# Performance work log

Hardware: AMD Instinct MI355X
Metric: run time of the kernel (lower is better)

## Reference

```python
import jax, jax.numpy as jnp
from jax import lax
import numpy as np

VOCAB, EMB, HID = 6, 64, 64


def _glorot(key, shape):
    fan_in, fan_out = shape[0], shape[-1]
    lim = np.sqrt(6.0 / (fan_in + fan_out)).astype(np.float32)
    return jax.random.uniform(key, shape, jnp.float32, -lim, lim)


def setup_inputs() -> dict:
    key = jax.random.key(0)
    ks = jax.random.split(key, 10)
    B, T = 256, 2048
    tokens = jax.random.randint(ks[0], (B, T), 0, VOCAB, dtype=jnp.int32)
    emb = jax.random.normal(ks[1], (VOCAB, EMB), jnp.float32) * 0.05  # Keras uniform init approx
    # LSTM kernels: gate order i, f, c(g), o ; kernel [EMB,4H], recurrent [H,4H], bias [4H]
    W_f = _glorot(ks[2], (EMB, 4 * HID))
    U_f = _glorot(ks[3], (HID, 4 * HID))
    b_f = jnp.zeros((4 * HID,), jnp.float32).at[HID:2 * HID].set(1.0)  # unit_forget_bias
    W_b = _glorot(ks[4], (EMB, 4 * HID))
    U_b = _glorot(ks[5], (HID, 4 * HID))
    b_b = jnp.zeros((4 * HID,), jnp.float32).at[HID:2 * HID].set(1.0)
    W_d = _glorot(ks[6], (2 * HID, 1))
    b_d = jnp.zeros((1,), jnp.float32)
    return {"tokens": tokens, "emb": emb, "W_f": W_f, "U_f": U_f, "b_f": b_f,
            "W_b": W_b, "U_b": U_b, "b_b": b_b, "W_d": W_d, "b_d": b_d}


def _masked_lstm(x, mask, W, U, b):
    """x: [B,T,E] float, mask: [B,T] bool. Returns [B,T,H].
    Keras mask semantics: at masked steps, state AND output carry previous values."""
    B = x.shape[0]
    h0 = jnp.zeros((B, HID), x.dtype)
    c0 = jnp.zeros((B, HID), x.dtype)

    def step(carry, inp):
        h, c = carry
        xt, mt = inp  # [B,E], [B]
        z = xt @ W + h @ U + b  # [B,4H]
        i, f, g, o = jnp.split(z, 4, axis=-1)
        c_new = jax.nn.sigmoid(f) * c + jax.nn.sigmoid(i) * jnp.tanh(g)
        h_new = jax.nn.sigmoid(o) * jnp.tanh(c_new)
        m = mt[:, None]
        h2 = jnp.where(m, h_new, h)
        c2 = jnp.where(m, c_new, c)
        return (h2, c2), h2

    xs = (jnp.swapaxes(x, 0, 1), jnp.swapaxes(mask, 0, 1))  # time-major
    _, hs = lax.scan(step, (h0, c0), xs)
    return jnp.swapaxes(hs, 0, 1)  # [B,T,H]


def reference(tokens, emb, W_f, U_f, b_f, W_b, U_b, b_b, W_d, b_d):
    mask = tokens != 0  # mask_zero=True
    x = emb[tokens]  # [B,T,EMB]
    fwd = _masked_lstm(x, mask, W_f, U_f, b_f)
    # backward direction: reverse inputs and mask in time, run, reverse outputs back
    bwd = _masked_lstm(x[:, ::-1], mask[:, ::-1], W_b, U_b, b_b)[:, ::-1]
    seq = jnp.concatenate([fwd, bwd], axis=-1)  # [B,T,2H]
    last = seq[:, -1, :]
    return last @ W_d + b_d  # [B,1]
```

## Files before the change

### kernel.cpp

```cpp
#include <hip/hip_runtime.h>


#define TT 2048
#define L2E 1.4426950408889634f

__device__ __forceinline__ float fexp2(float x) { return __builtin_amdgcn_exp2f(x); }
__device__ __forceinline__ float frcp(float x)  { return __builtin_amdgcn_rcpf(x); }
__device__ __forceinline__ float fsigm(float x) { return frcp(1.f + fexp2(-L2E * x)); }
__device__ __forceinline__ float ftanh(float x) { return fmaf(2.f, frcp(1.f + fexp2(-2.f * L2E * x)), -1.f); }
__device__ __forceinline__ float readlane_f(float v, int l) {
  return __builtin_bit_cast(float, __builtin_amdgcn_readlane(__builtin_bit_cast(int, v), l));
}

__global__ void
__attribute__((amdgpu_flat_work_group_size(256, 256)))
__attribute__((amdgpu_waves_per_eu(1, 1)))
lstm_fused(
    const int* __restrict__ tokens,
    const float* __restrict__ emb,
    const float* __restrict__ W_f, const float* __restrict__ U_f, const float* __restrict__ b_f,
    const float* __restrict__ W_b, const float* __restrict__ b_b,
    const float* __restrict__ W_d, const float* __restrict__ b_d,
    float* __restrict__ out)
{
  const int b    = blockIdx.x;
  const int tid  = threadIdx.x;
  const int lane = tid & 63;
  const int g    = tid >> 6;

  __shared__ int   tok_s [TT + 8];
  __shared__ int   ctok_s[TT + 8];
  __shared__ float emb_s[6 * 64];
  __shared__ float zx_s [6 * 272];
  __shared__ float zxb_s[6 * 256];
  __shared__ float act_s[2][4 * 68];
  __shared__ int   wsum[4];

  {
    const int4* tsrc = (const int4*)(tokens + b * TT);
    int4* tdst = (int4*)tok_s;
    for (int i = tid; i < TT / 4; i += 256) tdst[i] = tsrc[i];
    if (tid < 8) { tok_s[TT + tid] = 0; ctok_s[TT + tid] = 0; }
    for (int i = tid; i < 384; i += 256) emb_s[i] = emb[i];
  }
  __syncthreads();

  int mytok[8];
  int cnt = 0;
#pragma unroll
  for (int j = 0; j < 8; ++j) {
    mytok[j] = tok_s[tid * 8 + j];
    cnt += (mytok[j] != 0);
  }
  int inc = cnt;
#pragma unroll
  for (int off = 1; off < 64; off <<= 1) {
    int v = __shfl_up(inc, off, 64);
    if (lane >= off) inc += v;
  }
  if (lane == 63) wsum[g] = inc;
  __syncthreads();
  int base = 0;
#pragma unroll
  for (int w = 0; w < 4; ++w) base += (w < g) ? wsum[w] : 0;
  int pos = base + inc - cnt;
#pragma unroll
  for (int j = 0; j < 8; ++j)
    if (mytok[j] != 0) ctok_s[pos++] = mytok[j];
  const int nact = __builtin_amdgcn_readfirstlane(wsum[0] + wsum[1] + wsum[2] + wsum[3]);

  {
    float af[6], ab[6];
#pragma unroll
    for (int v = 0; v < 6; ++v) { af[v] = b_f[tid]; ab[v] = b_b[tid]; }
    for (int e = 0; e < 64; ++e) {
      const float wf = W_f[e * 256 + tid];
      const float wb = W_b[e * 256 + tid];
#pragma unroll
      for (int v = 0; v < 6; ++v) {
        af[v] = fmaf(emb_s[v * 64 + e], wf, af[v]);
        ab[v] = fmaf(emb_s[v * 64 + e], wb, ab[v]);
      }
    }
#pragma unroll
    for (int v = 0; v < 6; ++v) {
      zx_s [v * 272 + g * 68 + lane] = af[v];
      zxb_s[v * 256 + tid] = ab[v];
    }
  }

  float Ucol[64];
#pragma unroll
  for (int k = 0; k < 64; ++k) Ucol[k] = U_f[k * 256 + tid];

  __syncthreads();

  const float m1 = (g == 2) ? (-2.f * L2E) : (-L2E);
  const float ya = (g == 2) ? 2.f : 1.f;
  const float yb = (g == 2) ? -1.f : 0.f;
  const int   goff = g * 68 + lane;

  float h_reg = 0.f, c_reg = 0.f;
  int   buf = 0;
  int   tokc = ctok_s[0];

  for (int s = 0; s < nact; ++s) {
    const int tokn = ctok_s[s + 1];
    const float zxv = zx_s[tokc * 272 + goff];
    float a0 = 0.f, a1 = 0.f, a2 = 0.f, a3 = 0.f;
#pragma unroll
    for (int k = 0; k < 64; k += 4) {
      a0 = fmaf(readlane_f(h_reg, k + 0), Ucol[k + 0], a0);
      a1 = fmaf(readlane_f(h_reg, k + 1), Ucol[k + 1], a1);
      a2 = fmaf(readlane_f(h_reg, k + 2), Ucol[k + 2], a2);
      a3 = fmaf(readlane_f(h_reg, k + 3), Ucol[k + 3], a3);
    }
    const float z = zxv + ((a0 + a1) + (a2 + a3));
    const float y = fmaf(ya, frcp(1.f + fexp2(z * m1)), yb);
    act_s[buf][goff] = y;
    __syncthreads();
    const float ai  = act_s[buf][lane];
    const float af2 = act_s[buf][68 + lane];
    const float ag  = act_s[buf][136 + lane];
    const float ao  = act_s[buf][204 + lane];
    c_reg = fmaf(af2, c_reg, ai * ag);
    h_reg = ao * ftanh(c_reg);
    buf ^= 1;
    tokc = tokn;
  }

  if (tid < 64) {
    const float hf   = h_reg;
    const int   tokL = tok_s[TT - 1];
    float hbv = 0.f;
    if (tokL != 0) {
      const float zi = zxb_s[tokL * 256 + tid];
      const float zg = zxb_s[tokL * 256 + 128 + tid];
      const float zo = zxb_s[tokL * 256 + 192 + tid];
      const float cn = fsigm(zi) * ftanh(zg);
      hbv = fsigm(zo) * ftanh(cn);
    }
    float pr = fmaf(hf, W_d[tid], hbv * W_d[64 + tid]);
#pragma unroll
    for (int off = 32; off > 0; off >>= 1) pr += __shfl_xor(pr, off, 64);
    if (tid == 0) out[b] = pr + b_d[0];
  }
}

extern "C" void kernel_launch(void* const* d_in, const int* in_sizes, int n_in,
                              void* d_out, int out_size, void* d_ws, size_t ws_size,
                              hipStream_t stream) {
  const int*   tokens = (const int*)d_in[0];
  const float* emb    = (const float*)d_in[1];
  const float* W_f    = (const float*)d_in[2];
  const float* U_f    = (const float*)d_in[3];
  const float* b_f    = (const float*)d_in[4];
  const float* W_b    = (const float*)d_in[5];
  const float* U_b    = (const float*)d_in[6];
  (void)U_b;
  const float* b_b    = (const float*)d_in[7];
  const float* W_d    = (const float*)d_in[8];
  const float* b_d    = (const float*)d_in[9];
  float* out = (float*)d_out;
  (void)d_ws; (void)ws_size;

  lstm_fused<<<256, 256, 0, stream>>>(tokens, emb, W_f, U_f, b_f, W_b, b_b,
                                      W_d, b_d, out);
}
```

Baseline: 770.1 us.

## Run each sequence's LSTM recurrence in a single wave without barriers

Moves each batch row from four waves (one per gate) to a single 64-lane wave. Each lane now computes all four gates for its hidden unit, using packed v2f FMAs over 128 U values held in registers. This removes the per-step __syncthreads and the LDS exchange of activations, and lets the per-step input projection be read as one float4. The cost is roughly four times the FMA work per lane per step and much higher register pressure (256 VGPRs for U), which could cause spills, while only one wave per CU is busy.

```diff
diff --git a/kernel.cpp b/kernel.cpp
--- a/kernel.cpp
+++ b/kernel.cpp
@@ -3,6 +3,8 @@
 
 #define TT 2048
 #define L2E 1.4426950408889634f
+
+typedef float v2f __attribute__((ext_vector_type(2)));
 
 __device__ __forceinline__ float fexp2(float x) { return __builtin_amdgcn_exp2f(x); }
 __device__ __forceinline__ float frcp(float x)  { return __builtin_amdgcn_rcpf(x); }
@@ -13,7 +15,7 @@
 }
 
 __global__ void
-__attribute__((amdgpu_flat_work_group_size(256, 256)))
+__attribute__((amdgpu_flat_work_group_size(64, 64)))
 __attribute__((amdgpu_waves_per_eu(1, 1)))
 lstm_fused(
     const int* __restrict__ tokens,
@@ -23,59 +25,49 @@
     const float* __restrict__ W_d, const float* __restrict__ b_d,
     float* __restrict__ out)
 {
-  const int b    = blockIdx.x;
-  const int tid  = threadIdx.x;
-  const int lane = tid & 63;
-  const int g    = tid >> 6;
+  const int b = blockIdx.x;
+  const int u = threadIdx.x;
 
-  __shared__ int   tok_s [TT + 8];
+  __shared__ int   tok_s [TT];
   __shared__ int   ctok_s[TT + 8];
   __shared__ float emb_s[6 * 64];
-  __shared__ float zx_s [6 * 272];
-  __shared__ float zxb_s[6 * 256];
-  __shared__ float act_s[2][4 * 68];
-  __shared__ int   wsum[4];
+  __shared__ float zx_s [6 * 256] __attribute__((aligned(16)));
+  __shared__ float zxb_s[6 * 256] __attribute__((aligned(16)));
 
   {
     const int4* tsrc = (const int4*)(tokens + b * TT);
     int4* tdst = (int4*)tok_s;
-    for (int i = tid; i < TT / 4; i += 256) tdst[i] = tsrc[i];
-    if (tid < 8) { tok_s[TT + tid] = 0; ctok_s[TT + tid] = 0; }
-    for (int i = tid; i < 384; i += 256) emb_s[i] = emb[i];
+    for (int i = u; i < TT / 4; i += 64) tdst[i] = tsrc[i];
+    for (int i = u; i < 384; i += 64) emb_s[i] = emb[i];
   }
   __syncthreads();
 
-  int mytok[8];
   int cnt = 0;
-#pragma unroll
-  for (int j = 0; j < 8; ++j) {
-    mytok[j] = tok_s[tid * 8 + j];
-    cnt += (mytok[j] != 0);
-  }
+  for (int j = 0; j < 32; ++j) cnt += (tok_s[u * 32 + j] != 0);
   int inc = cnt;
 #pragma unroll
   for (int off = 1; off < 64; off <<= 1) {
     int v = __shfl_up(inc, off, 64);
-    if (lane >= off) inc += v;
+    if (u >= off) inc += v;
   }
-  if (lane == 63) wsum[g] = inc;
+  int pos = inc - cnt;
+  for (int j = 0; j < 32; ++j) {
+    const int t = tok_s[u * 32 + j];
+    if (t != 0) ctok_s[pos++] = t;
+  }
+  const int nact = __builtin_amdgcn_readfirstlane(__shfl(inc, 63, 64));
+  if (u < 8) ctok_s[nact + u] = 0;
   __syncthreads();
-  int base = 0;
+
 #pragma unroll
-  for (int w = 0; w < 4; ++w) base += (w < g) ? wsum[w] : 0;
-  int pos = base + inc - cnt;
-#pragma unroll
-  for (int j = 0; j < 8; ++j)
-    if (mytok[j] != 0) ctok_s[pos++] = mytok[j];
-  const int nact = __builtin_amdgcn_readfirstlane(wsum[0] + wsum[1] + wsum[2] + wsum[3]);
-
-  {
+  for (int g4 = 0; g4 < 4; ++g4) {
+    const int col = g4 * 64 + u;
     float af[6], ab[6];
 #pragma unroll
-    for (int v = 0; v < 6; ++v) { af[v] = b_f[tid]; ab[v] = b_b[tid]; }
+    for (int v = 0; v < 6; ++v) { af[v] = b_f[col]; ab[v] = b_b[col]; }
     for (int e = 0; e < 64; ++e) {
-      const float wf = W_f[e * 256 + tid];
-      const float wb = W_b[e * 256 + tid];
+      const float wf = W_f[e * 256 + col];
+      const float wb = W_b[e * 256 + col];
 #pragma unroll
       for (int v = 0; v < 6; ++v) {
         af[v] = fmaf(emb_s[v * 64 + e], wf, af[v]);
@@ -84,67 +76,57 @@
     }
 #pragma unroll
     for (int v = 0; v < 6; ++v) {
-      zx_s [v * 272 + g * 68 + lane] = af[v];
-      zxb_s[v * 256 + tid] = ab[v];
+      zx_s [v * 256 + u * 4 + g4] = af[v];
+      zxb_s[v * 256 + u * 4 + g4] = ab[v];
     }
   }
 
-  float Ucol[64];
+  v2f U01[64], U23[64];
 #pragma unroll
-  for (int k = 0; k < 64; ++k) Ucol[k] = U_f[k * 256 + tid];
+  for (int k = 0; k < 64; ++k) {
+    U01[k] = v2f{U_f[k * 256 + u],       U_f[k * 256 + 64 + u]};
+    U23[k] = v2f{U_f[k * 256 + 128 + u], U_f[k * 256 + 192 + u]};
+  }
 
   __syncthreads();
 
-  const float m1 = (g == 2) ? (-2.f * L2E) : (-L2E);
-  const float ya = (g == 2) ? 2.f : 1.f;
-  const float yb = (g == 2) ? -1.f : 0.f;
-  const int   goff = g * 68 + lane;
-
   float h_reg = 0.f, c_reg = 0.f;
-  int   buf = 0;
-  int   tokc = ctok_s[0];
+  int tokc = ctok_s[0];
 
   for (int s = 0; s < nact; ++s) {
     const int tokn = ctok_s[s + 1];
-    const float zxv = zx_s[tokc * 272 + goff];
-    float a0 = 0.f, a1 = 0.f, a2 = 0.f, a3 = 0.f;
+    const float4 zx4 = *(const float4*)&zx_s[tokc * 256 + u * 4];
+    v2f a01 = v2f{zx4.x, zx4.y}, a23 = v2f{zx4.z, zx4.w};
+    v2f b01 = v2f{0.f, 0.f},     b23 = v2f{0.f, 0.f};
 #pragma unroll
-    for (int k = 0; k < 64; k += 4) {
-      a0 = fmaf(readlane_f(h_reg, k + 0), Ucol[k + 0], a0);
-      a1 = fmaf(readlane_f(h_reg, k + 1), Ucol[k + 1], a1);
-      a2 = fmaf(readlane_f(h_reg, k + 2), Ucol[k + 2], a2);
-      a3 = fmaf(readlane_f(h_reg, k + 3), Ucol[k + 3], a3);
+    for (int k = 0; k < 64; k += 2) {
+      const float h0 = readlane_f(h_reg, k);
+      const float h1 = readlane_f(h_reg, k + 1);
+      a01 += U01[k] * h0;       a23 += U23[k] * h0;
+      b01 += U01[k + 1] * h1;   b23 += U23[k + 1] * h1;
     }
-    const float z = zxv + ((a0 + a1) + (a2 + a3));
-    const float y = fmaf(ya, frcp(1.f + fexp2(z * m1)), yb);
-    act_s[buf][goff] = y;
-    __syncthreads();
-    const float ai  = act_s[buf][lane];
-    const float af2 = act_s[buf][68 + lane];
-    const float ag  = act_s[buf][136 + lane];
-    const float ao  = act_s[buf][204 + lane];
-    c_reg = fmaf(af2, c_reg, ai * ag);
-    h_reg = ao * ftanh(c_reg);
-    buf ^= 1;
+    const v2f z01 = a01 + b01;
+    const v2f z23 = a23 + b23;
+    const float yi = fsigm(z01.x);
+    const float yf = fsigm(z01.y);
+    const float yg = ftanh(z23.x);
+    const float yo = fsigm(z23.y);
+    c_reg = fmaf(yf, c_reg, yi * yg);
+    h_reg = yo * ftanh(c_reg);
     tokc = tokn;
   }
 
-  if (tid < 64) {
-    const float hf   = h_reg;
-    const int   tokL = tok_s[TT - 1];
-    float hbv = 0.f;
-    if (tokL != 0) {
-      const float zi = zxb_s[tokL * 256 + tid];
-      const float zg = zxb_s[tokL * 256 + 128 + tid];
-      const float zo = zxb_s[tokL * 256 + 192 + tid];
-      const float cn = fsigm(zi) * ftanh(zg);
-      hbv = fsigm(zo) * ftanh(cn);
-    }
-    float pr = fmaf(hf, W_d[tid], hbv * W_d[64 + tid]);
+  const int tokL = tok_s[TT - 1];
+  float hbv = 0.f;
+  if (tokL != 0) {
+    const float4 zb = *(const float4*)&zxb_s[tokL * 256 + u * 4];
+    const float cn = fsigm(zb.x) * ftanh(zb.z);
+    hbv = fsigm(zb.w) * ftanh(cn);
+  }
+  float pr = fmaf(h_reg, W_d[u], hbv * W_d[64 + u]);
 #pragma unroll
-    for (int off = 32; off > 0; off >>= 1) pr += __shfl_xor(pr, off, 64);
-    if (tid == 0) out[b] = pr + b_d[0];
-  }
+  for (int off = 32; off > 0; off >>= 1) pr += __shfl_xor(pr, off, 64);
+  if (u == 0) out[b] = pr + b_d[0];
 }
 
 extern "C" void kernel_launch(void* const* d_in, const int* in_sizes, int n_in,
@@ -164,6 +146,6 @@
   float* out = (float*)d_out;
   (void)d_ws; (void)ws_size;
 
-  lstm_fused<<<256, 256, 0, stream>>>(tokens, emb, W_f, U_f, b_f, W_b, b_b,
-                                      W_d, b_d, out);
+  lstm_fused<<<256, 64, 0, stream>>>(tokens, emb, W_f, U_f, b_f, W_b, b_b,
+                                     W_d, b_d, out);
 }
```

Result: slower. 1.328 ms (+72.4%).

## Remap LSTM gates within each wave and exchange activations via shuffles

Applied to the files above, without the earlier changes.

Each wave now owns 16 hidden units for all four gates instead of one gate for all 64 units. Gate activations are combined with in-wave shuffles, and only the new hidden state goes through LDS. This replaces the 256-float activation exchange and the redundant per-wave cell update with a 64-float h exchange, still behind one barrier per step. Readlanes are also batched into 16-wide buffers to overlap them with FMAs, which adds three cross-lane shuffles on the serial dependency chain.

```diff
diff --git a/kernel.cpp b/kernel.cpp
--- a/kernel.cpp
+++ b/kernel.cpp
@@ -11,6 +11,26 @@
 __device__ __forceinline__ float readlane_f(float v, int l) {
   return __builtin_bit_cast(float, __builtin_amdgcn_readlane(__builtin_bit_cast(int, v), l));
 }
+
+#define RL16(B, base)                                                             \
+  B[0]  = readlane_f(h_reg, (base) + 0);  B[1]  = readlane_f(h_reg, (base) + 1);  \
+  B[2]  = readlane_f(h_reg, (base) + 2);  B[3]  = readlane_f(h_reg, (base) + 3);  \
+  B[4]  = readlane_f(h_reg, (base) + 4);  B[5]  = readlane_f(h_reg, (base) + 5);  \
+  B[6]  = readlane_f(h_reg, (base) + 6);  B[7]  = readlane_f(h_reg, (base) + 7);  \
+  B[8]  = readlane_f(h_reg, (base) + 8);  B[9]  = readlane_f(h_reg, (base) + 9);  \
+  B[10] = readlane_f(h_reg, (base) + 10); B[11] = readlane_f(h_reg, (base) + 11); \
+  B[12] = readlane_f(h_reg, (base) + 12); B[13] = readlane_f(h_reg, (base) + 13); \
+  B[14] = readlane_f(h_reg, (base) + 14); B[15] = readlane_f(h_reg, (base) + 15);
+
+#define FMA16(B, base)                                                       \
+  a0 = fmaf(B[0],  Ucol[(base) + 0],  a0); a1 = fmaf(B[1],  Ucol[(base) + 1],  a1); \
+  a2 = fmaf(B[2],  Ucol[(base) + 2],  a2); a3 = fmaf(B[3],  Ucol[(base) + 3],  a3); \
+  a0 = fmaf(B[4],  Ucol[(base) + 4],  a0); a1 = fmaf(B[5],  Ucol[(base) + 5],  a1); \
+  a2 = fmaf(B[6],  Ucol[(base) + 6],  a2); a3 = fmaf(B[7],  Ucol[(base) + 7],  a3); \
+  a0 = fmaf(B[8],  Ucol[(base) + 8],  a0); a1 = fmaf(B[9],  Ucol[(base) + 9],  a1); \
+  a2 = fmaf(B[10], Ucol[(base) + 10], a2); a3 = fmaf(B[11], Ucol[(base) + 11], a3); \
+  a0 = fmaf(B[12], Ucol[(base) + 12], a0); a1 = fmaf(B[13], Ucol[(base) + 13], a1); \
+  a2 = fmaf(B[14], Ucol[(base) + 14], a2); a3 = fmaf(B[15], Ucol[(base) + 15], a3);
 
 __global__ void
 __attribute__((amdgpu_flat_work_group_size(256, 256)))
@@ -26,14 +46,18 @@
   const int b    = blockIdx.x;
   const int tid  = threadIdx.x;
   const int lane = tid & 63;
-  const int g    = tid >> 6;
+  const int w    = tid >> 6;
+  const int g    = lane >> 4;
+  const int ul   = lane & 15;
+  const int u    = 16 * w + ul;
+  const int col  = (g << 6) + u;
 
   __shared__ int   tok_s [TT + 8];
   __shared__ int   ctok_s[TT + 8];
   __shared__ float emb_s[6 * 64];
   __shared__ float zx_s [6 * 272];
   __shared__ float zxb_s[6 * 256];
-  __shared__ float act_s[2][4 * 68];
+  __shared__ float h_s[2][64];
   __shared__ int   wsum[4];
 
   {
@@ -42,6 +66,7 @@
     for (int i = tid; i < TT / 4; i += 256) tdst[i] = tsrc[i];
     if (tid < 8) { tok_s[TT + tid] = 0; ctok_s[TT + tid] = 0; }
     for (int i = tid; i < 384; i += 256) emb_s[i] = emb[i];
+    if (tid < 64) { h_s[0][tid] = 0.f; h_s[1][tid] = 0.f; }
   }
   __syncthreads();
 
@@ -58,11 +83,11 @@
     int v = __shfl_up(inc, off, 64);
     if (lane >= off) inc += v;
   }
-  if (lane == 63) wsum[g] = inc;
+  if (lane == 63) wsum[w] = inc;
   __syncthreads();
   int base = 0;
 #pragma unroll
-  for (int w = 0; w < 4; ++w) base += (w < g) ? wsum[w] : 0;
+  for (int ww = 0; ww < 4; ++ww) base += (ww < w) ? wsum[ww] : 0;
   int pos = base + inc - cnt;
 #pragma unroll
   for (int j = 0; j < 8; ++j)
@@ -84,23 +109,24 @@
     }
 #pragma unroll
     for (int v = 0; v < 6; ++v) {
-      zx_s [v * 272 + g * 68 + lane] = af[v];
+      zx_s [v * 272 + (tid >> 6) * 68 + (tid & 63)] = af[v];
       zxb_s[v * 256 + tid] = ab[v];
     }
   }
 
   float Ucol[64];
 #pragma unroll
-  for (int k = 0; k < 64; ++k) Ucol[k] = U_f[k * 256 + tid];
+  for (int k = 0; k < 64; ++k) Ucol[k] = U_f[k * 256 + col];
 
   __syncthreads();
 
   const float m1 = (g == 2) ? (-2.f * L2E) : (-L2E);
   const float ya = (g == 2) ? 2.f : 1.f;
   const float yb = (g == 2) ? -1.f : 0.f;
-  const int   goff = g * 68 + lane;
+  const int   goff = g * 68 + u;
 
-  float h_reg = 0.f, c_reg = 0.f;
+  float h_reg = 0.f;
+  float c_reg = 0.f;
   int   buf = 0;
   int   tokc = ctok_s[0];
 
@@ -108,24 +134,26 @@
     const int tokn = ctok_s[s + 1];
     const float zxv = zx_s[tokc * 272 + goff];
     float a0 = 0.f, a1 = 0.f, a2 = 0.f, a3 = 0.f;
-#pragma unroll
-    for (int k = 0; k < 64; k += 4) {
-      a0 = fmaf(readlane_f(h_reg, k + 0), Ucol[k + 0], a0);
-      a1 = fmaf(readlane_f(h_reg, k + 1), Ucol[k + 1], a1);
-      a2 = fmaf(readlane_f(h_reg, k + 2), Ucol[k + 2], a2);
-      a3 = fmaf(readlane_f(h_reg, k + 3), Ucol[k + 3], a3);
-    }
+    float hsA[16], hsB[16];
+    RL16(hsA, 0)
+    RL16(hsB, 16)
+    FMA16(hsA, 0)
+    RL16(hsA, 32)
+    FMA16(hsB, 16)
+    RL16(hsB, 48)
+    FMA16(hsA, 32)
+    FMA16(hsB, 48)
     const float z = zxv + ((a0 + a1) + (a2 + a3));
     const float y = fmaf(ya, frcp(1.f + fexp2(z * m1)), yb);
-    act_s[buf][goff] = y;
+    const float vf = __shfl(y, ul + 16, 64);
+    const float vg = __shfl(y, ul + 32, 64);
+    const float vo = __shfl(y, ul + 48, 64);
+    c_reg = fmaf(vf, c_reg, y * vg);
+    const float hn = vo * ftanh(c_reg);
+    if (lane < 16) h_s[buf ^ 1][u] = hn;
     __syncthreads();
-    const float ai  = act_s[buf][lane];
-    const float af2 = act_s[buf][68 + lane];
-    const float ag  = act_s[buf][136 + lane];
-    const float ao  = act_s[buf][204 + lane];
-    c_reg = fmaf(af2, c_reg, ai * ag);
-    h_reg = ao * ftanh(c_reg);
     buf ^= 1;
+    h_reg = h_s[buf][lane];
     tokc = tokn;
   }
 
```

Measured after the change: 861.8 us. 11.9% more time.
